# Kernel tuning notes

Hardware: AMD Instinct MI355X
Metric: run time of the kernel (lower is better)

Reference implementation:

```python
import jax, jax.numpy as jnp
import numpy as np

E = 2048        # embed_dim
HQ = 32         # num_query_heads
HKV = 8         # num_kv_heads
HD = E // HQ    # head_dim = 64
GROUP = HQ // HKV  # q_per_kv = 4
B, T = 2, 2048


def setup_inputs() -> dict:
    key = jax.random.key(0)
    ks = jax.random.split(key, 6)
    s = 0.02
    x  = jax.random.normal(ks[0], (B, T, E), dtype=jnp.float32)
    Wq = jax.random.normal(ks[1], (E, E), dtype=jnp.float32) * s
    Wk = jax.random.normal(ks[2], (E, HKV * HD), dtype=jnp.float32) * s
    Wv = jax.random.normal(ks[3], (E, HKV * HD), dtype=jnp.float32) * s
    Wo = jax.random.normal(ks[4], (E, E), dtype=jnp.float32) * s
    bo = jax.random.normal(ks[5], (E,), dtype=jnp.float32) * s
    return {"x": x, "Wq": Wq, "Wk": Wk, "Wv": Wv, "Wo": Wo, "bo": bo}


def reference(x, Wq, Wk, Wv, Wo, bo):
    Bc, Tc, _ = x.shape
    # projections
    q = (x @ Wq).reshape(Bc, Tc, HQ, HD).transpose(0, 2, 1, 3)      # [B,HQ,T,HD]
    k = (x @ Wk).reshape(Bc, Tc, HKV, HD).transpose(0, 2, 1, 3)     # [B,HKV,T,HD]
    v = (x @ Wv).reshape(Bc, Tc, HKV, HD).transpose(0, 2, 1, 3)     # [B,HKV,T,HD]
    # group queries by kv head instead of repeating k/v: [B,HKV,GROUP,T,HD]
    qg = q.reshape(Bc, HKV, GROUP, Tc, HD)
    scale = 1.0 / jnp.sqrt(jnp.asarray(HD, dtype=x.dtype))
    scores = jnp.einsum('bhgqd,bhkd->bhgqk', qg, k) * scale         # [B,HKV,GROUP,T,T]
    weights = jax.nn.softmax(scores, axis=-1)
    attn = jnp.einsum('bhgqk,bhkd->bhgqd', weights, v)              # [B,HKV,GROUP,T,HD]
    out = attn.reshape(Bc, HQ, Tc, HD).transpose(0, 2, 1, 3).reshape(Bc, Tc, E)
    return out @ Wo + bo
```

## Files before the change

kernel.cpp:

```cpp
#include <hip/hip_runtime.h>
#include <hip/hip_bf16.h>
#include <stdint.h>

#define E_ 2048
#define HQ_ 32
#define HKV_ 8
#define HD_ 64
#define B_ 2
#define T_ 2048
#define MROWS (B_*T_)
#define NKV (HKV_*HD_)
#define NQKV (E_ + 2*NKV)
#define SCALE_LOG2E 0.18033688011112042f

typedef __bf16 bf16_t;
typedef __bf16 bf16x8 __attribute__((ext_vector_type(8)));
typedef float f32x4 __attribute__((ext_vector_type(4)));
typedef float f32x16 __attribute__((ext_vector_type(16)));

typedef const __attribute__((address_space(1))) unsigned int glb_u32;
typedef __attribute__((address_space(3))) unsigned int lds_u32;

__device__ __forceinline__ unsigned short f2bf_bits(float f) {
  unsigned int u = __float_as_uint(f);
  u += 0x7FFFu + ((u >> 16) & 1u);
  return (unsigned short)(u >> 16);
}
__device__ __forceinline__ bf16_t f2bf(float f) {
  union { unsigned short s; bf16_t h; } u;
  u.s = f2bf_bits(f);
  return u.h;
}
__device__ __forceinline__ unsigned pack2bf(float lo, float hi) {
  union { struct { bf16_t l, h; } s; unsigned u; } c;
  c.s.l = (bf16_t)lo; c.s.h = (bf16_t)hi;
  return c.u;
}
__device__ __forceinline__ float fexp2(float x) {
#if __has_builtin(__builtin_amdgcn_exp2f)
  return __builtin_amdgcn_exp2f(x);
#else
  return exp2f(x);
#endif
}

__global__ void cast_x_kernel(const float* __restrict__ in, bf16_t* __restrict__ out, int n8) {
  int i = blockIdx.x * blockDim.x + threadIdx.x;
  int stride = gridDim.x * blockDim.x;
  for (; i < n8; i += stride) {
    const float4* p = reinterpret_cast<const float4*>(in) + (size_t)i * 2;
    float4 a = p[0], b = p[1];
    union { unsigned short s[8]; uint4 v; } u;
    u.s[0] = f2bf_bits(a.x); u.s[1] = f2bf_bits(a.y);
    u.s[2] = f2bf_bits(a.z); u.s[3] = f2bf_bits(a.w);
    u.s[4] = f2bf_bits(b.x); u.s[5] = f2bf_bits(b.y);
    u.s[6] = f2bf_bits(b.z); u.s[7] = f2bf_bits(b.w);
    reinterpret_cast<uint4*>(out)[i] = u.v;
  }
}

__global__ void transpose_cast_w(const float* __restrict__ in, bf16_t* __restrict__ out,
                                 int R, int C) {
  __shared__ float tile[32][33];
  int c0 = blockIdx.x * 32, r0 = blockIdx.y * 32;
  int tx = threadIdx.x, ty = threadIdx.y;
#pragma unroll
  for (int j = 0; j < 4; ++j) {
    int r = ty + j * 8;
    tile[r][tx] = in[(size_t)(r0 + r) * C + c0 + tx];
  }
  __syncthreads();
#pragma unroll
  for (int j = 0; j < 4; ++j) {
    int c = ty + j * 8;
    out[(size_t)(c0 + c) * R + r0 + tx] = f2bf(tile[tx][c]);
  }
}

__global__ void transpose_v_kernel(const bf16_t* __restrict__ qkv, bf16_t* __restrict__ vt) {
  __shared__ bf16_t tile[32][33];
  int b = blockIdx.z;
  int hd0 = blockIdx.x * 32, t0 = blockIdx.y * 32;
  int tx = threadIdx.x, ty = threadIdx.y;
#pragma unroll
  for (int j = 0; j < 4; ++j) {
    int tt = ty + j * 8;
    tile[tt][tx] = qkv[(size_t)(b * T_ + t0 + tt) * NQKV + (E_ + NKV) + hd0 + tx];
  }
  __syncthreads();
#pragma unroll
  for (int j = 0; j < 4; ++j) {
    int hh = ty + j * 8;
    vt[(size_t)(b * NKV + hd0 + hh) * T_ + t0 + tx] = tile[tx][hh];
  }
}

#define VMW(n) asm volatile("s_waitcnt vmcnt(" #n ")" ::: "memory")
#define BARSYNC do { asm volatile("" ::: "memory");            \
                     __builtin_amdgcn_s_barrier();             \
                     asm volatile("" ::: "memory"); } while (0)

template <int BN, int OUTMODE>
__global__ __launch_bounds__(512, 2)
void gemm8_kernel(const bf16_t* __restrict__ A, const bf16_t* __restrict__ BT,
                  void* __restrict__ Cv, const float* __restrict__ bias,
                  int M, int N, int K) {
  constexpr int BM = 256, BK = 64;
  constexpr int WN = BN / 4;
  constexpr int ACN = (BN == 256) ? 4 : 2;
  __shared__ bf16_t As[2][BM * BK];
  __shared__ bf16_t Bs[2][BN * BK];

  const int tid = threadIdx.x;
  const int wid = tid >> 6, lane = tid & 63;
  const int l15 = lane & 15, l4 = lane >> 4;
  const int wr = wid >> 2, wc = wid & 3;
  const int m0 = blockIdx.x * BM, n0 = blockIdx.y * BN;
  const int srow = lane >> 3;
  const int schunk = (lane & 7) ^ srow;

  f32x4 acc[8][ACN];
  f32x4 zero = {0.f, 0.f, 0.f, 0.f};
#pragma unroll
  for (int i = 0; i < 8; ++i)
#pragma unroll
    for (int j = 0; j < ACN; ++j) acc[i][j] = zero;

#define STAGE_A(nb, h, ktt) do {                                                        \
    int k0s = (ktt) * BK;                                                               \
    _Pragma("unroll") for (int j = 0; j < 2; ++j) {                                     \
      int row0 = (h) * 64 + j * 128 + wid * 8;                                          \
      __builtin_amdgcn_global_load_lds(                                                 \
          (glb_u32*)(A + (size_t)(m0 + row0 + srow) * K + k0s + schunk * 8),            \
          (lds_u32*)(&As[nb][row0 * 64]), 16, 0, 0);                                    \
    } } while (0)

#define STAGE_B2(nb, h, ktt) do {                                                       \
    int k0s = (ktt) * BK;                                                               \
    _Pragma("unroll") for (int j = 0; j < 2; ++j) {                                     \
      int i0 = j * 64 + wid * 8;                                                        \
      int row0 = (i0 & 31) + ((i0 >> 5) << 6) + (h) * 32;                               \
      __builtin_amdgcn_global_load_lds(                                                 \
          (glb_u32*)(BT + (size_t)(n0 + row0 + srow) * K + k0s + schunk * 8),           \
          (lds_u32*)(&Bs[nb][row0 * 64]), 16, 0, 0);                                    \
    } } while (0)

#define STAGE_B1(nb, ktt) do {                                                          \
    int k0s = (ktt) * BK;                                                               \
    _Pragma("unroll") for (int j = 0; j < 2; ++j) {                                     \
      int row0 = j * 64 + wid * 8;                                                      \
      __builtin_amdgcn_global_load_lds(                                                 \
          (glb_u32*)(BT + (size_t)(n0 + row0 + srow) * K + k0s + schunk * 8),           \
          (lds_u32*)(&Bs[nb][row0 * 64]), 16, 0, 0);                                    \
    } } while (0)

  bf16x8 afr[4][2], bfr[2][2];
#define LDA(mh) { _Pragma("unroll") for (int mf = 0; mf < 4; ++mf)                      \
    _Pragma("unroll") for (int ks = 0; ks < 2; ++ks) {                                  \
      int row = wr * 128 + (mh) * 64 + mf * 16 + l15;                                   \
      afr[mf][ks] = *(const bf16x8*)&As[cur][row * 64 + ((ks * 4 + l4) ^ (l15 & 7)) * 8]; } }

#define LDB(nh) { _Pragma("unroll") for (int nf = 0; nf < 2; ++nf)                      \
    _Pragma("unroll") for (int ks = 0; ks < 2; ++ks) {                                  \
      int row = wc * WN + (nh) * 32 + nf * 16 + l15;                                    \
      bfr[nf][ks] = *(const bf16x8*)&Bs[cur][row * 64 + ((ks * 4 + l4) ^ (l15 & 7)) * 8]; } }

#define MMA(mh, nh) {                                                                   \
    __builtin_amdgcn_s_setprio(1);                                                      \
    _Pragma("unroll") for (int ks = 0; ks < 2; ++ks)                                    \
      _Pragma("unroll") for (int mf = 0; mf < 4; ++mf)                                  \
        _Pragma("unroll") for (int nf = 0; nf < 2; ++nf)                                \
          acc[(mh) * 4 + mf][(nh) * 2 + nf] = __builtin_amdgcn_mfma_f32_16x16x32_bf16(  \
              afr[mf][ks], bfr[nf][ks], acc[(mh) * 4 + mf][(nh) * 2 + nf], 0, 0, 0);    \
    __builtin_amdgcn_s_setprio(0); }

  const int nK = K >> 6;

  if (BN == 256) {
    STAGE_A(0, 0, 0); STAGE_B2(0, 0, 0); STAGE_B2(0, 1, 0); STAGE_A(0, 1, 0);
    VMW(4);
  } else {
    STAGE_A(0, 0, 0); STAGE_B1(0, 0);    STAGE_A(0, 1, 0);
    VMW(2);
  }
  BARSYNC;

  for (int kt = 0; kt < nK; ++kt) {
    const int cur = kt & 1, nb = cur ^ 1;
    const int ktn = (kt + 1 < nK) ? kt + 1 : 0;

    if (BN == 256) {
      LDA(0); LDB(0);
      STAGE_A(nb, 0, ktn);
      BARSYNC; MMA(0, 0); VMW(4); BARSYNC;
      LDB(1);
      STAGE_B2(nb, 0, ktn);
      BARSYNC; MMA(0, 1); VMW(4); BARSYNC;
      LDA(1);
      STAGE_B2(nb, 1, ktn);
      BARSYNC; MMA(1, 1); BARSYNC;
      LDB(0);
      STAGE_A(nb, 1, ktn);
      BARSYNC; MMA(1, 0); VMW(4); BARSYNC;
    } else {
      LDA(0); LDB(0);
      STAGE_A(nb, 0, ktn); STAGE_B1(nb, ktn);
      BARSYNC; MMA(0, 0); VMW(4); BARSYNC;
      LDA(1);
      STAGE_A(nb, 1, ktn);
      BARSYNC; MMA(1, 0); VMW(2); BARSYNC;
    }
  }
  VMW(0);

#pragma unroll
  for (int mq = 0; mq < 8; ++mq)
#pragma unroll
    for (int nq = 0; nq < ACN; ++nq) {
      int mrow = m0 + wr * 128 + (mq >> 2) * 64 + (mq & 3) * 16 + l4 * 4;
      int ncol = n0 + wc * WN + (nq >> 1) * 32 + (nq & 1) * 16 + l15;
      if (OUTMODE == 0) {
        bf16_t* C = reinterpret_cast<bf16_t*>(Cv);
#pragma unroll
        for (int r = 0; r < 4; ++r)
          C[(size_t)(mrow + r) * N + ncol] = f2bf(acc[mq][nq][r]);
      } else {
        float* C = reinterpret_cast<float*>(Cv);
        float bb = bias[ncol];
#pragma unroll
        for (int r = 0; r < 4; ++r)
          C[(size_t)(mrow + r) * N + ncol] = acc[mq][nq][r] + bb;
      }
    }
#undef STAGE_A
#undef STAGE_B2
#undef STAGE_B1
#undef LDA
#undef LDB
#undef MMA
}

__global__ void attn_kernel(const bf16_t* __restrict__ qkv, const bf16_t* __restrict__ vt,
                            bf16_t* __restrict__ attn) {
  __shared__ bf16_t Kbuf[2][64 * 64];
  __shared__ bf16_t Vbuf[2][64 * 64];
  __shared__ float bcast[8][32];

  int tid = threadIdx.x;
  int w = tid >> 6, lane = tid & 63;
  int l31 = lane & 31, hi = lane >> 5;
  int bh = blockIdx.y;
  int b = bh >> 5, hq = bh & 31, hkv = hq >> 2;
  int q0 = blockIdx.x * 256 + w * 32;

  bf16x8 qf[4];
  {
    const bf16_t* qp = qkv + (size_t)(b * T_ + q0 + l31) * NQKV + hq * HD_;
#pragma unroll
    for (int s = 0; s < 4; ++s) {
      bf16x8 q = *reinterpret_cast<const bf16x8*>(qp + s * 16 + hi * 8);
#pragma unroll
      for (int e = 0; e < 8; ++e) q[e] = (bf16_t)((float)q[e] * SCALE_LOG2E);
      qf[s] = q;
    }
  }

  f32x16 o0 = {0.f,0.f,0.f,0.f,0.f,0.f,0.f,0.f,0.f,0.f,0.f,0.f,0.f,0.f,0.f,0.f};
  f32x16 o1 = o0;
  float m_r = -1e30f, l_r = 0.f;

  int srow = w * 8 + (lane >> 3);
  int schunk = (lane & 7) ^ ((lane >> 3) & 7);
  const bf16_t* kg = qkv + (size_t)b * T_ * NQKV + E_ + hkv * HD_;
  const bf16_t* vg = vt + ((size_t)(b * HKV_ + hkv) * HD_ + srow) * T_;

#define STAGE_KV(bi, kv0) do {                                                          \
    __builtin_amdgcn_global_load_lds(                                                   \
        (glb_u32*)(kg + (size_t)((kv0) + srow) * NQKV + schunk * 8),                    \
        (lds_u32*)(&Kbuf[bi][w * 8 * 64]), 16, 0, 0);                                   \
    __builtin_amdgcn_global_load_lds(                                                   \
        (glb_u32*)(vg + (kv0) + schunk * 8),                                            \
        (lds_u32*)(&Vbuf[bi][w * 8 * 64]), 16, 0, 0);                                   \
  } while (0)

#define KREAD(bi, tsub, s) \
  (*reinterpret_cast<const bf16x8*>(&Kbuf[bi][((tsub) * 32 + l31) * 64 + \
      ((((s) * 2 + hi) ^ (l31 & 7)) * 8)]))
#define VREAD(bi, dh, s) \
  (*reinterpret_cast<const bf16x8*>(&Vbuf[bi][((dh) * 32 + l31) * 64 + \
      ((((s) * 2 + hi) ^ (l31 & 7)) * 8)]))

  STAGE_KV(0, 0);
  __syncthreads();

#pragma unroll 2
  for (int t = 0; t < T_ / 64; ++t) {
    int bi = t & 1;
    if (t < T_ / 64 - 1) STAGE_KV(bi ^ 1, (t + 1) * 64);

    f32x16 sa = {0.f,0.f,0.f,0.f,0.f,0.f,0.f,0.f,0.f,0.f,0.f,0.f,0.f,0.f,0.f,0.f};
    f32x16 sb = sa;
    __builtin_amdgcn_s_setprio(1);
#pragma unroll
    for (int s = 0; s < 4; ++s) {
      sa = __builtin_amdgcn_mfma_f32_32x32x16_bf16(KREAD(bi, 0, s), qf[s], sa, 0, 0, 0);
      sb = __builtin_amdgcn_mfma_f32_32x32x16_bf16(KREAD(bi, 1, s), qf[s], sb, 0, 0, 0);
    }
    __builtin_amdgcn_s_setprio(0);

    float pmax = sa[0];
#pragma unroll
    for (int r = 1; r < 16; ++r) pmax = fmaxf(pmax, sa[r]);
#pragma unroll
    for (int r = 0; r < 16; ++r) pmax = fmaxf(pmax, sb[r]);

    if (__any(pmax > m_r + 8.f)) {
      float pm2 = __shfl_xor(pmax, 32);
      float mnew = fmaxf(m_r, fmaxf(pmax, pm2));
      float corr = fexp2(m_r - mnew);
      m_r = mnew;
      l_r *= corr;
      bcast[w][l31] = corr;
      asm volatile("s_waitcnt lgkmcnt(0)" ::: "memory");
#pragma unroll
      for (int r = 0; r < 16; ++r) {
        float c = bcast[w][(r & 3) + 8 * (r >> 2) + 4 * hi];
        o0[r] *= c; o1[r] *= c;
      }
    }

    float pA[16], pB[16];
    float ps0 = 0.f, ps1 = 0.f;
#pragma unroll
    for (int r = 0; r < 16; ++r) {
      pA[r] = fexp2(sa[r] - m_r); ps0 += pA[r];
      pB[r] = fexp2(sb[r] - m_r); ps1 += pB[r];
    }
    l_r += ps0 + ps1;

    unsigned wd[2][4][2];
#pragma unroll
    for (int g = 0; g < 4; ++g)
#pragma unroll
      for (int j = 0; j < 2; ++j) {
        wd[0][g][j] = pack2bf(pA[4 * g + 2 * j], pA[4 * g + 2 * j + 1]);
        wd[1][g][j] = pack2bf(pB[4 * g + 2 * j], pB[4 * g + 2 * j + 1]);
      }

    __builtin_amdgcn_s_setprio(1);
#pragma unroll
    for (int s = 0; s < 4; ++s) {
      const int tt = s >> 1, gg = 2 * (s & 1);
      unsigned send0 = hi ? wd[tt][gg][0] : wd[tt][gg + 1][0];
      unsigned send1 = hi ? wd[tt][gg][1] : wd[tt][gg + 1][1];
      unsigned recv0 = __shfl_xor(send0, 32);
      unsigned recv1 = __shfl_xor(send1, 32);
      union { unsigned u[4]; bf16x8 v; } pf;
      pf.u[0] = hi ? recv0 : wd[tt][gg][0];
      pf.u[1] = hi ? recv1 : wd[tt][gg][1];
      pf.u[2] = hi ? wd[tt][gg + 1][0] : recv0;
      pf.u[3] = hi ? wd[tt][gg + 1][1] : recv1;
      o0 = __builtin_amdgcn_mfma_f32_32x32x16_bf16(pf.v, VREAD(bi, 0, s), o0, 0, 0, 0);
      o1 = __builtin_amdgcn_mfma_f32_32x32x16_bf16(pf.v, VREAD(bi, 1, s), o1, 0, 0, 0);
    }
    __builtin_amdgcn_s_setprio(0);

    __syncthreads();
  }
#undef STAGE_KV
#undef KREAD
#undef VREAD

  float lfull = l_r + __shfl_xor(l_r, 32);
  bcast[w][l31] = 1.0f / lfull;
  asm volatile("s_waitcnt lgkmcnt(0)" ::: "memory");
  const size_t obase = (size_t)(b * T_ + q0) * E_ + hq * HD_;
#pragma unroll
  for (int r = 0; r < 16; ++r) {
    int q = (r & 3) + 8 * (r >> 2) + 4 * hi;
    float rl = bcast[w][q];
    attn[obase + (size_t)q * E_ + l31]      = (bf16_t)(o0[r] * rl);
    attn[obase + (size_t)q * E_ + 32 + l31] = (bf16_t)(o1[r] * rl);
  }
}

extern "C" void kernel_launch(void* const* d_in, const int* in_sizes, int n_in,
                              void* d_out, int out_size, void* d_ws, size_t ws_size,
                              hipStream_t stream) {
  const float* x  = (const float*)d_in[0];
  const float* Wq = (const float*)d_in[1];
  const float* Wk = (const float*)d_in[2];
  const float* Wv = (const float*)d_in[3];
  const float* Wo = (const float*)d_in[4];
  const float* bo = (const float*)d_in[5];
  float* out = (float*)d_out;

  bf16_t* xb    = (bf16_t*)d_ws;
  bf16_t* WcatT = xb + (size_t)MROWS * E_;
  bf16_t* WoT   = WcatT + (size_t)NQKV * E_;
  bf16_t* QKV   = WoT + (size_t)E_ * E_;
  bf16_t* Vt    = QKV + (size_t)MROWS * NQKV;
  bf16_t* Attn  = Vt + (size_t)B_ * NKV * T_;

  dim3 tblk(32, 8);
  cast_x_kernel<<<2048, 256, 0, stream>>>(x, xb, MROWS * E_ / 8);
  transpose_cast_w<<<dim3(E_ / 32, E_ / 32), tblk, 0, stream>>>(Wq, WcatT, E_, E_);
  transpose_cast_w<<<dim3(NKV / 32, E_ / 32), tblk, 0, stream>>>(Wk, WcatT + (size_t)E_ * E_, E_, NKV);
  transpose_cast_w<<<dim3(NKV / 32, E_ / 32), tblk, 0, stream>>>(Wv, WcatT + (size_t)(E_ + NKV) * E_, E_, NKV);
  transpose_cast_w<<<dim3(E_ / 32, E_ / 32), tblk, 0, stream>>>(Wo, WoT, E_, E_);

  gemm8_kernel<256, 0><<<dim3(MROWS / 256, NQKV / 256), 512, 0, stream>>>(
      xb, WcatT, (void*)QKV, nullptr, MROWS, NQKV, E_);

  transpose_v_kernel<<<dim3(NKV / 32, T_ / 32, B_), tblk, 0, stream>>>(QKV, Vt);

  attn_kernel<<<dim3(T_ / 256, B_ * HQ_), 512, 0, stream>>>(QKV, Vt, Attn);

  gemm8_kernel<128, 1><<<dim3(MROWS / 256, E_ / 128), 512, 0, stream>>>(
      Attn, WoT, (void*)out, bo, MROWS, E_, E_);
}
```

Measured before the change: 375.2 us.

## Shrink attention blocks to four waves, tree-reduce softmax, reorder GEMM staging

The attention kernel drops from 8 to 4 waves per block (128 queries per block, twice as many blocks). Each wave now stages two 8-row slices of K/V into LDS. The per-lane max and sum reductions become tree reductions to shorten the dependency chains. In the QKV GEMM, prefetch loads for the next k-tile are issued earlier, with adjusted vmcnt waits, to overlap more memory latency. In exchange, each K/V tile is loaded from global memory twice as many times across blocks, and there are fewer waves per block to hide latency.

```diff
diff --git a/kernel.cpp b/kernel.cpp
--- a/kernel.cpp
+++ b/kernel.cpp
@@ -191,16 +191,15 @@
 
     if (BN == 256) {
       LDA(0); LDB(0);
-      STAGE_A(nb, 0, ktn);
-      BARSYNC; MMA(0, 0); VMW(4); BARSYNC;
+      STAGE_A(nb, 0, ktn); STAGE_B2(nb, 0, ktn);
+      BARSYNC; MMA(0, 0); VMW(6); BARSYNC;
       LDB(1);
-      STAGE_B2(nb, 0, ktn);
-      BARSYNC; MMA(0, 1); VMW(4); BARSYNC;
+      STAGE_B2(nb, 1, ktn);
+      BARSYNC; MMA(0, 1); VMW(6); BARSYNC;
       LDA(1);
-      STAGE_B2(nb, 1, ktn);
+      STAGE_A(nb, 1, ktn);
       BARSYNC; MMA(1, 1); BARSYNC;
       LDB(0);
-      STAGE_A(nb, 1, ktn);
       BARSYNC; MMA(1, 0); VMW(4); BARSYNC;
     } else {
       LDA(0); LDB(0);
@@ -244,14 +243,14 @@
                             bf16_t* __restrict__ attn) {
   __shared__ bf16_t Kbuf[2][64 * 64];
   __shared__ bf16_t Vbuf[2][64 * 64];
-  __shared__ float bcast[8][32];
+  __shared__ float bcast[4][32];
 
   int tid = threadIdx.x;
   int w = tid >> 6, lane = tid & 63;
   int l31 = lane & 31, hi = lane >> 5;
   int bh = blockIdx.y;
   int b = bh >> 5, hq = bh & 31, hkv = hq >> 2;
-  int q0 = blockIdx.x * 256 + w * 32;
+  int q0 = blockIdx.x * 128 + w * 32;
 
   bf16x8 qf[4];
   {
@@ -269,19 +268,21 @@
   f32x16 o1 = o0;
   float m_r = -1e30f, l_r = 0.f;
 
-  int srow = w * 8 + (lane >> 3);
-  int schunk = (lane & 7) ^ ((lane >> 3) & 7);
+  int srow = lane >> 3;
+  int schunk = (lane & 7) ^ srow;
   const bf16_t* kg = qkv + (size_t)b * T_ * NQKV + E_ + hkv * HD_;
-  const bf16_t* vg = vt + ((size_t)(b * HKV_ + hkv) * HD_ + srow) * T_;
+  const bf16_t* vg = vt + (size_t)(b * HKV_ + hkv) * HD_ * T_;
 
 #define STAGE_KV(bi, kv0) do {                                                          \
-    __builtin_amdgcn_global_load_lds(                                                   \
-        (glb_u32*)(kg + (size_t)((kv0) + srow) * NQKV + schunk * 8),                    \
-        (lds_u32*)(&Kbuf[bi][w * 8 * 64]), 16, 0, 0);                                   \
-    __builtin_amdgcn_global_load_lds(                                                   \
-        (glb_u32*)(vg + (kv0) + schunk * 8),                                            \
-        (lds_u32*)(&Vbuf[bi][w * 8 * 64]), 16, 0, 0);                                   \
-  } while (0)
+    _Pragma("unroll") for (int half = 0; half < 2; ++half) {                            \
+      int r0 = w * 16 + half * 8;                                                       \
+      __builtin_amdgcn_global_load_lds(                                                 \
+          (glb_u32*)(kg + (size_t)((kv0) + r0 + srow) * NQKV + schunk * 8),             \
+          (lds_u32*)(&Kbuf[bi][r0 * 64]), 16, 0, 0);                                    \
+      __builtin_amdgcn_global_load_lds(                                                 \
+          (glb_u32*)(vg + (size_t)(r0 + srow) * T_ + (kv0) + schunk * 8),               \
+          (lds_u32*)(&Vbuf[bi][r0 * 64]), 16, 0, 0);                                    \
+    } } while (0)
 
 #define KREAD(bi, tsub, s) \
   (*reinterpret_cast<const bf16x8*>(&Kbuf[bi][((tsub) * 32 + l31) * 64 + \
@@ -308,11 +309,15 @@
     }
     __builtin_amdgcn_s_setprio(0);
 
-    float pmax = sa[0];
-#pragma unroll
-    for (int r = 1; r < 16; ++r) pmax = fmaxf(pmax, sa[r]);
-#pragma unroll
-    for (int r = 0; r < 16; ++r) pmax = fmaxf(pmax, sb[r]);
+    float tm[16];
+#pragma unroll
+    for (int r = 0; r < 16; ++r) tm[r] = fmaxf(sa[r], sb[r]);
+#pragma unroll
+    for (int off = 8; off >= 1; off >>= 1)
+#pragma unroll
+      for (int r = 0; r < 8; ++r)
+        if (r < off) tm[r] = fmaxf(tm[r], tm[r + off]);
+    float pmax = tm[0];
 
     if (__any(pmax > m_r + 8.f)) {
       float pm2 = __shfl_xor(pmax, 32);
@@ -329,14 +334,19 @@
       }
     }
 
-    float pA[16], pB[16];
-    float ps0 = 0.f, ps1 = 0.f;
+    float pA[16], pB[16], ts[16];
 #pragma unroll
     for (int r = 0; r < 16; ++r) {
-      pA[r] = fexp2(sa[r] - m_r); ps0 += pA[r];
-      pB[r] = fexp2(sb[r] - m_r); ps1 += pB[r];
-    }
-    l_r += ps0 + ps1;
+      pA[r] = fexp2(sa[r] - m_r);
+      pB[r] = fexp2(sb[r] - m_r);
+      ts[r] = pA[r] + pB[r];
+    }
+#pragma unroll
+    for (int off = 8; off >= 1; off >>= 1)
+#pragma unroll
+      for (int r = 0; r < 8; ++r)
+        if (r < off) ts[r] += ts[r + off];
+    l_r += ts[0];
 
     unsigned wd[2][4][2];
 #pragma unroll
@@ -414,7 +424,7 @@
 
   transpose_v_kernel<<<dim3(NKV / 32, T_ / 32, B_), tblk, 0, stream>>>(QKV, Vt);
 
-  attn_kernel<<<dim3(T_ / 256, B_ * HQ_), 512, 0, stream>>>(QKV, Vt, Attn);
+  attn_kernel<<<dim3(T_ / 128, B_ * HQ_), 256, 0, stream>>>(QKV, Vt, Attn);
 
   gemm8_kernel<128, 1><<<dim3(MROWS / 256, E_ / 128), 512, 0, stream>>>(
       Attn, WoT, (void*)out, bo, MROWS, E_, E_);
```

New measurement: 400.3 us. 1.07x slower.
